# Kernel optimization log

Hardware: AMD Instinct MI355X
Metric: run time of the kernel (lower is better)

## Reference

```python
import jax, jax.numpy as jnp
import numpy as np

N_NODES = 50000
N_EDGES = 640000
D = 128
BN_EPS = 1e-5


def setup_inputs() -> dict:
    key = jax.random.key(0)
    k1, k2, k3 = jax.random.split(key, 3)
    x = jax.random.normal(k1, (N_NODES, D), dtype=jnp.float32)
    # Glorot-ish weight for GCNConv linear
    W = jax.random.normal(k2, (D, D), dtype=jnp.float32) * (1.0 / np.sqrt(D))
    b = jnp.zeros((D,), dtype=jnp.float32)
    gamma = jnp.ones((D,), dtype=jnp.float32)
    beta = jnp.zeros((D,), dtype=jnp.float32)
    edge_index = jax.random.randint(k3, (2, N_EDGES), 0, N_NODES, dtype=jnp.int64)
    return {"x": x, "W": W, "b": b, "gamma": gamma, "beta": beta, "edge_index": edge_index}


def reference(x, W, b, gamma, beta, edge_index):
    N = x.shape[0]
    # --- GCNConv: x' = D^{-1/2} (A + I) D^{-1/2} (x W) + b ---
    xw = x @ W  # [N, D]
    loops = jnp.arange(N, dtype=edge_index.dtype)
    src = jnp.concatenate([edge_index[0], loops])  # [E+N]
    dst = jnp.concatenate([edge_index[1], loops])
    ones = jnp.ones(src.shape[0], dtype=x.dtype)
    deg = jax.ops.segment_sum(ones, dst, num_segments=N)  # in-degree incl. self-loop
    dinv = jnp.where(deg > 0, jax.lax.rsqrt(deg), 0.0)
    norm = dinv[src] * dinv[dst]  # [E+N]
    msg = xw[src] * norm[:, None]  # [E+N, D] gathered + scaled messages
    h = jax.ops.segment_sum(msg, dst, num_segments=N) + b  # scatter-add aggregation
    # --- BatchNorm1d (training-mode batch stats over nodes, biased var) ---
    mean = jnp.mean(h, axis=0)
    var = jnp.mean(jnp.square(h - mean), axis=0)
    h = (h - mean) * jax.lax.rsqrt(var + BN_EPS) * gamma + beta
    # --- activation (relu) ---
    h = jax.nn.relu(h)
    # --- residual (in_channels == out_channels) ---
    h = x + h
    # --- dropout: identity in eval mode for deterministic reference ---
    return h
```

## Files before the change

### kernel.cpp

```cpp
#include <hip/hip_runtime.h>

#define DCH 128
#define ROWS 16
#define BN_EPS 1e-5f

typedef unsigned short u16;
typedef __attribute__((ext_vector_type(8))) short short8;
typedef __attribute__((ext_vector_type(4))) float floatx4;
typedef __attribute__((ext_vector_type(2))) unsigned uint2v;

__device__ __forceinline__ float bf2f(u16 u) {
    return __uint_as_float(((unsigned)u) << 16);
}
__device__ __forceinline__ u16 f2bf(float f) {
    unsigned u = __float_as_uint(f);
    u += 0x7FFFu + ((u >> 16) & 1u);
    return (u16)(u >> 16);
}
__device__ __forceinline__ float ldf(const void* p, int i, int isbf) {
    return isbf ? bf2f(((const u16*)p)[i]) : ((const float*)p)[i];
}

__global__ void zero_kernel(float* p, int n) {
    int stride = gridDim.x * 256;
    for (int i = blockIdx.x * 256 + threadIdx.x; i < n; i += stride) p[i] = 0.f;
}

__global__ void paint_kernel(u16* out, int n, unsigned val) {
    int stride = gridDim.x * 256;
    for (int i = blockIdx.x * 256 + threadIdx.x; i < n; i += stride) out[i] = (u16)val;
}

__global__ void prep_deg_kernel(const int* ei, int E, const u16* xw, int* ws_i,
                                const void* W, u16* Wb, int* deg, int N) {
    int t = threadIdx.x;
    __shared__ int s_nz, s_hits;
    if (t == 0) { s_nz = 0; s_hits = 0; }
    __syncthreads();
    int ewords = 2 * E;
    int nz = 0;
    for (int i = t; i < 1024; i += 256) {
        int w = 2 * i + 1;
        if (w < ewords) nz |= ei[w];
    }
    if (nz) atomicOr(&s_nz, 1);
    unsigned m = (xw[2 * t] >> 8) & 0x7F;
    if (m >= 0x3B && m <= 0x43) atomicAdd(&s_hits, 1);
    __syncthreads();
    int is64 = (s_nz == 0) ? 1 : 0;
    int isbf = (s_hits >= 128) ? 1 : 0;
    if (blockIdx.x == 0 && t == 0) {
        ws_i[0] = is64;
        ws_i[1] = isbf;
    }
    int gid = blockIdx.x * 256 + t;
    int gthreads = gridDim.x * 256;
    for (int idx = gid; idx < DCH * DCH; idx += gthreads) {
        int j = idx & 7, lane = (idx >> 3) & 63, kk = (idx >> 9) & 3, nt = idx >> 11;
        int k = kk * 32 + (lane >> 4) * 8 + j;
        int n = nt * 16 + (lane & 15);
        Wb[idx] = f2bf(ldf(W, k * DCH + n, isbf));
    }
    if (is64 && !(E & 1)) {
        int P2 = E >> 1;
        for (int p = gid; p < P2; p += gthreads) {
            int4 sp = ((const int4*)ei)[p];
            int4 dp = ((const int4*)(ei + 2 * E))[p];
            if (((unsigned)sp.x >= (unsigned)N) || ((unsigned)dp.x >= (unsigned)N) ||
                ((unsigned)sp.z >= (unsigned)N) || ((unsigned)dp.z >= (unsigned)N))
                atomicOr(&ws_i[2], 2);
            atomicAdd(&deg[min(max(dp.x, 0), N - 1)], 1);
            atomicAdd(&deg[min(max(dp.z, 0), N - 1)], 1);
        }
    } else {
        for (int e = gid; e < E; e += gthreads) {
            int s = is64 ? ei[2 * e] : ei[e];
            int d = is64 ? ei[2 * E + 2 * e] : ei[E + e];
            if (((unsigned)s >= (unsigned)N) || ((unsigned)d >= (unsigned)N))
                atomicOr(&ws_i[2], 2);
            atomicAdd(&deg[min(max(d, 0), N - 1)], 1);
        }
    }
}

__global__ void detect_kernel(const int* ei, int ewords, const u16* xw, int* ws_i) {
    __shared__ int s_nz, s_hits;
    int t = threadIdx.x;
    if (t == 0) { s_nz = 0; s_hits = 0; }
    __syncthreads();
    int nz = 0;
    for (int i = t; i < 1024; i += 256) {
        int w = 2 * i + 1;
        if (w < ewords) nz |= ei[w];
    }
    if (nz) atomicOr(&s_nz, 1);
    unsigned m = (xw[2 * t] >> 8) & 0x7F;
    if (m >= 0x3B && m <= 0x43) atomicAdd(&s_hits, 1);
    __syncthreads();
    if (t == 0) {
        ws_i[0] = (s_nz == 0) ? 1 : 0;
        ws_i[1] = (s_hits >= 128) ? 1 : 0;
        ws_i[2] = 0;
    }
}

__global__ void deg_kernel(const int* ei, int E, int* ws_i, int* deg, int N) {
    int is64 = ws_i[0];
    int i = blockIdx.x * 256 + threadIdx.x;
    if (i < E) {
        int s = is64 ? ei[2 * i] : ei[i];
        int d = is64 ? ei[2 * E + 2 * i] : ei[E + i];
        if (((unsigned)s >= (unsigned)N) || ((unsigned)d >= (unsigned)N))
            atomicOr(&ws_i[2], 2);
        d = min(max(d, 0), N - 1);
        atomicAdd(&deg[d], 1);
    }
}

__global__ void dinv_kernel(const int* deg, float* dinv, int N, int* ws_i) {
    int i = blockIdx.x * 256 + threadIdx.x;
    if (i < N) {
        float v = rsqrtf((float)(deg[i] + 1));
        if (!(v > 0.f && v <= 1.001f)) atomicOr(&ws_i[2], 4);
        dinv[i] = v;
    }
}

__global__ void scanA_kernel(const int* deg, int* part, int N) {
    int base = blockIdx.x * 1024 + threadIdx.x * 4;
    int s = 0;
    #pragma unroll
    for (int j = 0; j < 4; ++j) {
        int i = base + j;
        if (i < N) s += deg[i];
    }
    #pragma unroll
    for (int o = 1; o < 64; o <<= 1) s += __shfl_xor(s, o, 64);
    __shared__ int ws4[4];
    if ((threadIdx.x & 63) == 0) ws4[threadIdx.x >> 6] = s;
    __syncthreads();
    if (threadIdx.x == 0) part[blockIdx.x] = ws4[0] + ws4[1] + ws4[2] + ws4[3];
}

__global__ void scanC_kernel(int* deg_cursor, const int* part, int* rowptr,
                             float* dinv, int N, int P) {
    __shared__ int wsum[4], wsP[4];
    int t = threadIdx.x, lane = t & 63, w = t >> 6;
    int pv = (t < P && t < (int)blockIdx.x) ? part[t] : 0;
    #pragma unroll
    for (int o = 1; o < 64; o <<= 1) pv += __shfl_xor(pv, o, 64);
    if (lane == 0) wsP[w] = pv;

    int base = blockIdx.x * 1024 + t * 4;
    int v[4], ts = 0;
    #pragma unroll
    for (int j = 0; j < 4; ++j) {
        int i = base + j;
        v[j] = (i < N) ? deg_cursor[i] : 0;
        ts += v[j];
    }
    int sc = ts;
    #pragma unroll
    for (int o = 1; o < 64; o <<= 1) {
        int u = __shfl_up(sc, o, 64);
        if (lane >= o) sc += u;
    }
    if (lane == 63) wsum[w] = sc;
    __syncthreads();
    if (t < 4) {
        int s = wsum[t];
        #pragma unroll
        for (int o = 1; o < 4; o <<= 1) {
            int u = __shfl_up(s, o, 4);
            if (t >= o) s += u;
        }
        wsum[t] = s;
    }
    __syncthreads();
    int blockbase = wsP[0] + wsP[1] + wsP[2] + wsP[3];
    int run = sc - ts + (w ? wsum[w - 1] : 0) + blockbase;
    #pragma unroll
    for (int j = 0; j < 4; ++j) {
        int i = base + j;
        if (i < N) {
            deg_cursor[i] = run;
            run += v[j];
            rowptr[i + 1] = run;
            dinv[i] = rsqrtf((float)(v[j] + 1));
        }
    }
    if (blockIdx.x == 0 && t == 0) rowptr[0] = 0;
}

__global__ void fillcsr_kernel(const int* ei, int E, const int* ws_i,
                               int* cursor, int* col, int N) {
    int is64 = ws_i[0];
    int i = blockIdx.x * 256 + threadIdx.x;
    if (is64 && !(E & 1)) {
        if (2 * i < E) {
            int4 sp = ((const int4*)ei)[i];
            int4 dp = ((const int4*)(ei + 2 * E))[i];
            int s0 = min(max(sp.x, 0), N - 1), d0 = min(max(dp.x, 0), N - 1);
            int s1 = min(max(sp.z, 0), N - 1), d1 = min(max(dp.z, 0), N - 1);
            int p0 = atomicAdd(&cursor[d0], 1);
            if ((unsigned)p0 < (unsigned)E) col[p0] = s0;
            int p1 = atomicAdd(&cursor[d1], 1);
            if ((unsigned)p1 < (unsigned)E) col[p1] = s1;
        }
    } else if (i < E) {
        int s = is64 ? ei[2 * i] : ei[i];
        int d = is64 ? ei[2 * E + 2 * i] : ei[E + i];
        s = min(max(s, 0), N - 1);
        d = min(max(d, 0), N - 1);
        int pos = atomicAdd(&cursor[d], 1);
        if ((unsigned)pos < (unsigned)E) col[pos] = s;
    }
}

__global__ void gemm_mfma_kernel(const void* x, const u16* Wb, const float* dinv,
                                 const int* ws_i, u16* y, int N) {
    int isbf = ws_i[1];
    int t = threadIdx.x;
    int wv = t >> 6, lane = t & 63;
    int quad = lane >> 4, l16 = lane & 15;
    int r0 = blockIdx.x * 64 + wv * 16;
    int rl = min(r0 + l16, N - 1);
    short8 a[4];
    if (isbf) {
        const u16* xp = (const u16*)x + (size_t)rl * DCH + quad * 8;
        #pragma unroll
        for (int kk = 0; kk < 4; ++kk)
            a[kk] = *(const short8*)(xp + kk * 32);
    } else {
        const float* xp = (const float*)x + (size_t)rl * DCH + quad * 8;
        #pragma unroll
        for (int kk = 0; kk < 4; ++kk) {
            float4 f0 = *(const float4*)(xp + kk * 32);
            float4 f1 = *(const float4*)(xp + kk * 32 + 4);
            short8 aa;
            aa[0] = (short)f2bf(f0.x); aa[1] = (short)f2bf(f0.y);
            aa[2] = (short)f2bf(f0.z); aa[3] = (short)f2bf(f0.w);
            aa[4] = (short)f2bf(f1.x); aa[5] = (short)f2bf(f1.y);
            aa[6] = (short)f2bf(f1.z); aa[7] = (short)f2bf(f1.w);
            a[kk] = aa;
        }
    }
    floatx4 acc[8];
    #pragma unroll
    for (int i = 0; i < 8; ++i) acc[i] = (floatx4)(0.f);
    #pragma unroll
    for (int nt = 0; nt < 8; ++nt) {
        #pragma unroll
        for (int kk = 0; kk < 4; ++kk) {
            short8 bfr = *(const short8*)&Wb[(((nt << 2) | kk) * 64 + lane) * 8];
            acc[nt] = __builtin_amdgcn_mfma_f32_16x16x32_bf16(a[kk], bfr, acc[nt], 0, 0, 0);
        }
    }
    #pragma unroll
    for (int i = 0; i < 4; ++i) {
        int row = r0 + quad * 4 + i;
        if (row < N) {
            float dv = dinv[row];
            #pragma unroll
            for (int nt = 0; nt < 8; ++nt)
                y[(size_t)row * DCH + nt * 16 + l16] = f2bf(acc[nt][i] * dv);
        }
    }
}

__global__ __launch_bounds__(256, 4)
void gather_stats_kernel(const int* rowptr, const int* col, const u16* y,
                         const float* dinv, const void* b, const int* ws_i,
                         float* h, float* sums, float* sumsq, int N) {
    int isbf = ws_i[1];
    int t = threadIdx.x;
    int hw = t >> 5;
    int l32 = t & 31;
    int c0 = l32 * 4;
    float bb[4];
    #pragma unroll
    for (int k = 0; k < 4; ++k) bb[k] = ldf(b, c0 + k, isbf);
    float ps[4] = {0.f, 0.f, 0.f, 0.f}, pq[4] = {0.f, 0.f, 0.f, 0.f};
    int stream_id = blockIdx.x * 8 + hw;
    int nstreams = gridDim.x * 8;

    int n = stream_id;
    int beg = 0, end = 0;
    uint2v qs = (uint2v)(0u);
    if (n < N) {
        beg = rowptr[n];
        end = rowptr[n + 1];
        qs = *(const uint2v*)&y[(size_t)n * DCH + c0];
    }
    while (n < N) {
        int n2 = n + nstreams;
        int begN = 0, endN = 0;
        uint2v qsN = (uint2v)(0u);
        if (n2 < N) {
            begN = rowptr[n2];
            endN = rowptr[n2 + 1];
            qsN = *(const uint2v*)&y[(size_t)n2 * DCH + c0];
        }

        float a0[4] = { bf2f((u16)(qs.x & 0xFFFF)), bf2f((u16)(qs.x >> 16)),
                        bf2f((u16)(qs.y & 0xFFFF)), bf2f((u16)(qs.y >> 16)) };
        float a1[4] = {0.f, 0.f, 0.f, 0.f};
        float a2[4] = {0.f, 0.f, 0.f, 0.f};
        float a3[4] = {0.f, 0.f, 0.f, 0.f};
        int j = beg;
        int s0 = 0, s1 = 0, s2 = 0, s3 = 0, s4 = 0, s5 = 0, s6 = 0, s7 = 0;
        bool have8 = (j + 7 < end);
        if (have8) {
            s0 = __builtin_nontemporal_load(col + j);
            s1 = __builtin_nontemporal_load(col + j + 1);
            s2 = __builtin_nontemporal_load(col + j + 2);
            s3 = __builtin_nontemporal_load(col + j + 3);
            s4 = __builtin_nontemporal_load(col + j + 4);
            s5 = __builtin_nontemporal_load(col + j + 5);
            s6 = __builtin_nontemporal_load(col + j + 6);
            s7 = __builtin_nontemporal_load(col + j + 7);
        }
        while (have8) {
            uint2v q0 = *(const uint2v*)&y[(size_t)s0 * DCH + c0];
            uint2v q1 = *(const uint2v*)&y[(size_t)s1 * DCH + c0];
            uint2v q2 = *(const uint2v*)&y[(size_t)s2 * DCH + c0];
            uint2v q3 = *(const uint2v*)&y[(size_t)s3 * DCH + c0];
            uint2v q4 = *(const uint2v*)&y[(size_t)s4 * DCH + c0];
            uint2v q5 = *(const uint2v*)&y[(size_t)s5 * DCH + c0];
            uint2v q6 = *(const uint2v*)&y[(size_t)s6 * DCH + c0];
            uint2v q7 = *(const uint2v*)&y[(size_t)s7 * DCH + c0];
            int jn = j + 8;
            bool haven = (jn + 7 < end);
            if (haven) {
                s0 = __builtin_nontemporal_load(col + jn);
                s1 = __builtin_nontemporal_load(col + jn + 1);
                s2 = __builtin_nontemporal_load(col + jn + 2);
                s3 = __builtin_nontemporal_load(col + jn + 3);
                s4 = __builtin_nontemporal_load(col + jn + 4);
                s5 = __builtin_nontemporal_load(col + jn + 5);
                s6 = __builtin_nontemporal_load(col + jn + 6);
                s7 = __builtin_nontemporal_load(col + jn + 7);
            }
            a0[0] += bf2f((u16)(q0.x & 0xFFFF)); a0[1] += bf2f((u16)(q0.x >> 16));
            a0[2] += bf2f((u16)(q0.y & 0xFFFF)); a0[3] += bf2f((u16)(q0.y >> 16));
            a1[0] += bf2f((u16)(q1.x & 0xFFFF)); a1[1] += bf2f((u16)(q1.x >> 16));
            a1[2] += bf2f((u16)(q1.y & 0xFFFF)); a1[3] += bf2f((u16)(q1.y >> 16));
            a2[0] += bf2f((u16)(q2.x & 0xFFFF)); a2[1] += bf2f((u16)(q2.x >> 16));
            a2[2] += bf2f((u16)(q2.y & 0xFFFF)); a2[3] += bf2f((u16)(q2.y >> 16));
            a3[0] += bf2f((u16)(q3.x & 0xFFFF)); a3[1] += bf2f((u16)(q3.x >> 16));
            a3[2] += bf2f((u16)(q3.y & 0xFFFF)); a3[3] += bf2f((u16)(q3.y >> 16));
            a0[0] += bf2f((u16)(q4.x & 0xFFFF)); a0[1] += bf2f((u16)(q4.x >> 16));
            a0[2] += bf2f((u16)(q4.y & 0xFFFF)); a0[3] += bf2f((u16)(q4.y >> 16));
            a1[0] += bf2f((u16)(q5.x & 0xFFFF)); a1[1] += bf2f((u16)(q5.x >> 16));
            a1[2] += bf2f((u16)(q5.y & 0xFFFF)); a1[3] += bf2f((u16)(q5.y >> 16));
            a2[0] += bf2f((u16)(q6.x & 0xFFFF)); a2[1] += bf2f((u16)(q6.x >> 16));
            a2[2] += bf2f((u16)(q6.y & 0xFFFF)); a2[3] += bf2f((u16)(q6.y >> 16));
            a3[0] += bf2f((u16)(q7.x & 0xFFFF)); a3[1] += bf2f((u16)(q7.x >> 16));
            a3[2] += bf2f((u16)(q7.y & 0xFFFF)); a3[3] += bf2f((u16)(q7.y >> 16));
            j = jn; have8 = haven;
        }
        if (j + 3 < end) {
            s0 = __builtin_nontemporal_load(col + j);
            s1 = __builtin_nontemporal_load(col + j + 1);
            s2 = __builtin_nontemporal_load(col + j + 2);
            s3 = __builtin_nontemporal_load(col + j + 3);
            uint2v q0 = *(const uint2v*)&y[(size_t)s0 * DCH + c0];
            uint2v q1 = *(const uint2v*)&y[(size_t)s1 * DCH + c0];
            uint2v q2 = *(const uint2v*)&y[(size_t)s2 * DCH + c0];
            uint2v q3 = *(const uint2v*)&y[(size_t)s3 * DCH + c0];
            a0[0] += bf2f((u16)(q0.x & 0xFFFF)); a0[1] += bf2f((u16)(q0.x >> 16));
            a0[2] += bf2f((u16)(q0.y & 0xFFFF)); a0[3] += bf2f((u16)(q0.y >> 16));
            a1[0] += bf2f((u16)(q1.x & 0xFFFF)); a1[1] += bf2f((u16)(q1.x >> 16));
            a1[2] += bf2f((u16)(q1.y & 0xFFFF)); a1[3] += bf2f((u16)(q1.y >> 16));
            a2[0] += bf2f((u16)(q2.x & 0xFFFF)); a2[1] += bf2f((u16)(q2.x >> 16));
            a2[2] += bf2f((u16)(q2.y & 0xFFFF)); a2[3] += bf2f((u16)(q2.y >> 16));
            a3[0] += bf2f((u16)(q3.x & 0xFFFF)); a3[1] += bf2f((u16)(q3.x >> 16));
            a3[2] += bf2f((u16)(q3.y & 0xFFFF)); a3[3] += bf2f((u16)(q3.y >> 16));
            j += 4;
        }
        for (; j < end; ++j) {
            uint2v q0 = *(const uint2v*)&y[(size_t)__builtin_nontemporal_load(col + j) * DCH + c0];
            a0[0] += bf2f((u16)(q0.x & 0xFFFF)); a0[1] += bf2f((u16)(q0.x >> 16));
            a0[2] += bf2f((u16)(q0.y & 0xFFFF)); a0[3] += bf2f((u16)(q0.y >> 16));
        }
        float dn = dinv[n];
        floatx4 o;
        o[0] = fmaf((a0[0] + a1[0]) + (a2[0] + a3[0]), dn, bb[0]);
        o[1] = fmaf((a0[1] + a1[1]) + (a2[1] + a3[1]), dn, bb[1]);
        o[2] = fmaf((a0[2] + a1[2]) + (a2[2] + a3[2]), dn, bb[2]);
        o[3] = fmaf((a0[3] + a1[3]) + (a2[3] + a3[3]), dn, bb[3]);
        __builtin_nontemporal_store(o, (floatx4*)&h[(size_t)n * DCH + c0]);
        ps[0] += o[0]; pq[0] += o[0] * o[0];
        ps[1] += o[1]; pq[1] += o[1] * o[1];
        ps[2] += o[2]; pq[2] += o[2] * o[2];
        ps[3] += o[3]; pq[3] += o[3] * o[3];

        n = n2; beg = begN; end = endN; qs = qsN;
    }
    __shared__ float lps[8][DCH], lpq[8][DCH];
    #pragma unroll
    for (int k = 0; k < 4; ++k) { lps[hw][c0 + k] = ps[k]; lpq[hw][c0 + k] = pq[k]; }
    __syncthreads();
    if (t < DCH) {
        int ch = (t + blockIdx.x * 16) & 127;
        float s = 0.f, q = 0.f;
        #pragma unroll
        for (int i = 0; i < 8; ++i) { s += lps[i][ch]; q += lpq[i][ch]; }
        atomicAdd(&sums[ch], s);
        atomicAdd(&sumsq[ch], q);
    }
}

__global__ void gemm_valu_kernel(const void* x, const void* W, const float* dinv,
                                 const int* ws_i, void* y, int N) {
    __shared__ float WsF[64 * DCH];
    __shared__ float xs[ROWS * DCH];
    int isbf = ws_i[1];
    int t = threadIdx.x;
    int r0 = blockIdx.x * ROWS;
    for (int i = t; i < ROWS * DCH; i += 256) {
        int r = r0 + (i >> 7);
        xs[i] = (r < N) ? ldf(x, r * DCH + (i & 127), isbf) : 0.f;
    }
    int d = t & 127, rh = t >> 7;
    float s[8];
    #pragma unroll
    for (int j = 0; j < 8; ++j) s[j] = 0.f;
    for (int half = 0; half < 2; ++half) {
        __syncthreads();
        for (int i = t; i < 64 * DCH; i += 256)
            WsF[i] = ldf(W, half * 64 * DCH + i, isbf);
        __syncthreads();
        #pragma unroll
        for (int j = 0; j < 8; ++j) {
            int rr = rh + 2 * j;
            float a = s[j];
            #pragma unroll 16
            for (int k = 0; k < 64; ++k)
                a = fmaf(xs[rr * DCH + half * 64 + k], WsF[k * DCH + d], a);
            s[j] = a;
        }
    }
    #pragma unroll
    for (int j = 0; j < 8; ++j) {
        int r = r0 + rh + 2 * j;
        if (r < N) {
            float v = s[j] * dinv[r];
            if (isbf) ((u16*)y)[r * DCH + d] = f2bf(v);
            else      ((float*)y)[r * DCH + d] = v;
        }
    }
}

__global__ void scatter_kernel(const int* ei, int E, const int* ws_i,
                               const void* y, float* acc, int N) {
    int is64 = ws_i[0], isbf = ws_i[1];
    int gid = blockIdx.x * 256 + threadIdx.x;
    int e = gid >> 5;
    if (e >= E) return;
    int c0 = (gid & 31) * 4;
    int s = is64 ? ei[2 * e] : ei[e];
    int d = is64 ? ei[2 * E + 2 * e] : ei[E + e];
    s = min(max(s, 0), N - 1);
    d = min(max(d, 0), N - 1);
    float v0, v1, v2, v3;
    if (isbf) {
        uint2 raw = *(const uint2*)&((const u16*)y)[s * DCH + c0];
        v0 = bf2f((u16)(raw.x & 0xFFFF)); v1 = bf2f((u16)(raw.x >> 16));
        v2 = bf2f((u16)(raw.y & 0xFFFF)); v3 = bf2f((u16)(raw.y >> 16));
    } else {
        float4 raw = *(const float4*)&((const float*)y)[s * DCH + c0];
        v0 = raw.x; v1 = raw.y; v2 = raw.z; v3 = raw.w;
    }
    float* a = &acc[d * DCH + c0];
    atomicAdd(a + 0, v0);
    atomicAdd(a + 1, v1);
    atomicAdd(a + 2, v2);
    atomicAdd(a + 3, v3);
}

__global__ void bnstat_kernel(const void* y, float* acc, const float* dinv,
                              const void* b, int* ws_i,
                              float* sums, float* sumsq, int total) {
    int isbf = ws_i[1];
    int t = threadIdx.x;
    int d = t & 127;
    float bb = ldf(b, d, isbf);
    float ps = 0.f, pq = 0.f;
    int stride = gridDim.x * 256;
    for (int i = blockIdx.x * 256 + t; i < total; i += stride) {
        int r = i >> 7;
        float yv = isbf ? bf2f(((const u16*)y)[i]) : ((const float*)y)[i];
        float v = (yv + acc[i]) * dinv[r] + bb;
        acc[i] = v;
        ps += v;
        pq += v * v;
    }
    __shared__ float ls[256], lq[256];
    ls[t] = ps; lq[t] = pq;
    __syncthreads();
    if (t < 128) {
        atomicAdd(&sums[d], ls[t] + ls[t + 128]);
        atomicAdd(&sumsq[d], lq[t] + lq[t + 128]);
    }
}

__global__ void out_kernel(const float* h, const void* x,
                           const void* gamma, const void* beta,
                           int* ws_i, const float* sums, const float* sumsq,
                           void* out, int total, float invN) {
    __shared__ float sc[DCH], sh[DCH];
    int isbf = ws_i[1];
    int t = threadIdx.x;
    if (t < DCH) {
        float mean = sums[t] * invN;
        float var = fmaxf(sumsq[t] * invN - mean * mean, 0.f);
        float s = ldf(gamma, t, isbf) * rsqrtf(var + BN_EPS);
        if (!(var < 1e8f && fabsf(s) < 1e6f)) atomicOr(&ws_i[2], 32);
        sc[t] = s;
        sh[t] = ldf(beta, t, isbf) - mean * s;
    }
    __syncthreads();
    int total4 = total >> 2;
    int stride = gridDim.x * 256;
    int i0 = blockIdx.x * 256 + t;
    int d0 = (i0 << 2) & 127;
    float c0 = sc[d0], c1 = sc[d0 + 1], c2 = sc[d0 + 2], c3 = sc[d0 + 3];
    float f0 = sh[d0], f1 = sh[d0 + 1], f2 = sh[d0 + 2], f3 = sh[d0 + 3];
    if (isbf) {
        for (int i = i0; i < total4; i += stride) {
            floatx4 hv = __builtin_nontemporal_load((const floatx4*)h + i);
            uint2v xv = __builtin_nontemporal_load((const uint2v*)x + i);
            float v0 = fmaxf(fmaf(hv[0], c0, f0), 0.f) + bf2f((u16)(xv.x & 0xFFFF));
            float v1 = fmaxf(fmaf(hv[1], c1, f1), 0.f) + bf2f((u16)(xv.x >> 16));
            float v2 = fmaxf(fmaf(hv[2], c2, f2), 0.f) + bf2f((u16)(xv.y & 0xFFFF));
            float v3 = fmaxf(fmaf(hv[3], c3, f3), 0.f) + bf2f((u16)(xv.y >> 16));
            uint2v o;
            o.x = (unsigned)f2bf(v0) | ((unsigned)f2bf(v1) << 16);
            o.y = (unsigned)f2bf(v2) | ((unsigned)f2bf(v3) << 16);
            __builtin_nontemporal_store(o, (uint2v*)out + i);
        }
    } else {
        for (int i = i0; i < total4; i += stride) {
            floatx4 hv = __builtin_nontemporal_load((const floatx4*)h + i);
            floatx4 xv = __builtin_nontemporal_load((const floatx4*)x + i);
            floatx4 o;
            o[0] = fmaxf(fmaf(hv[0], c0, f0), 0.f) + xv[0];
            o[1] = fmaxf(fmaf(hv[1], c1, f1), 0.f) + xv[1];
            o[2] = fmaxf(fmaf(hv[2], c2, f2), 0.f) + xv[2];
            o[3] = fmaxf(fmaf(hv[3], c3, f3), 0.f) + xv[3];
            __builtin_nontemporal_store(o, (floatx4*)out + i);
        }
    }
    for (int i = (total4 << 2) + i0; i < total; i += stride) {
        int d = i & 127;
        float v = fmaxf(fmaf(h[i], sc[d], sh[d]), 0.f);
        if (isbf) ((u16*)out)[i] = f2bf(v + bf2f(((const u16*)x)[i]));
        else      ((float*)out)[i] = v + ((const float*)x)[i];
    }
}

__global__ void diag_kernel(const int* ws_i, void* out, int n) {
    int e = ws_i[2];
    if (!e) return;
    int isbf = ws_i[1];
    float v = 4096.f + 32.f * (float)(e & 63);
    int stride = gridDim.x * 256;
    if (isbf) {
        u16 code = f2bf(v);
        for (int i = blockIdx.x * 256 + threadIdx.x; i < n; i += stride)
            ((u16*)out)[i] = code;
    } else {
        for (int i = blockIdx.x * 256 + threadIdx.x; i < n; i += stride)
            ((float*)out)[i] = v;
    }
}

extern "C" void kernel_launch(void* const* d_in, const int* in_sizes, int n_in,
                              void* d_out, int out_size, void* d_ws, size_t ws_size,
                              hipStream_t stream) {
    const void* x     = d_in[0];
    const void* W     = d_in[1];
    const void* b     = d_in[2];
    const void* gamma = d_in[3];
    const void* beta  = d_in[4];
    const int*  ei    = (const int*)d_in[5];

    const int N  = in_sizes[0] / DCH;
    const int E  = in_sizes[5] / 2;
    const int ND = N * DCH;
    const int P  = (N + 1023) / 1024;

    char* wsb = (char*)d_ws;
    int*  ws_i = (int*)wsb;

    size_t o_wb   = 64;
    size_t o_deg  = o_wb + 32768;
    size_t o_sum  = o_deg + 4 * (size_t)N;
    size_t o_sq   = o_sum + 512;
    size_t o_rp   = o_sq + 512;
    size_t o_dinv = o_rp + 4 * ((size_t)N + 1) + 4;
    size_t o_part = o_dinv + 4 * (size_t)N;
    size_t o_h    = (o_part + 1024 + 255) & ~(size_t)255;
    size_t o_col  = o_h + 4 * (size_t)ND;
    size_t need_csr = o_col + 4 * (size_t)E;

    (void)hipGetLastError();

    if (ws_size >= need_csr && P <= 256) {
        u16*   Wb    = (u16*)(wsb + o_wb);
        int*   deg   = (int*)(wsb + o_deg);
        float* sums  = (float*)(wsb + o_sum);
        float* sumsq = (float*)(wsb + o_sq);
        int*   rowptr= (int*)(wsb + o_rp);
        float* dinv  = (float*)(wsb + o_dinv);
        int*   part  = (int*)(wsb + o_part);
        float* h     = (float*)(wsb + o_h);
        int*   col   = (int*)(wsb + o_col);
        u16*   y     = (u16*)d_out;

        zero_kernel<<<128, 256, 0, stream>>>((float*)wsb, (int)((o_sq + 512) / 4));
        prep_deg_kernel<<<1250, 256, 0, stream>>>(ei, E, (const u16*)x, ws_i,
                                                  W, Wb, deg, N);
        scanA_kernel<<<P, 256, 0, stream>>>(deg, part, N);
        scanC_kernel<<<P, 256, 0, stream>>>(deg, part, rowptr, dinv, N, P);
        fillcsr_kernel<<<(E + 255) / 256, 256, 0, stream>>>(ei, E, ws_i, deg, col, N);
        gemm_mfma_kernel<<<(N + 63) / 64, 256, 0, stream>>>(x, Wb, dinv, ws_i, y, N);
        gather_stats_kernel<<<1024, 256, 0, stream>>>(rowptr, col, y, dinv, b, ws_i,
                                                      h, sums, sumsq, N);
        out_kernel<<<2048, 256, 0, stream>>>(h, x, gamma, beta, ws_i, sums, sumsq,
                                             d_out, ND, 1.0f / (float)N);
        diag_kernel<<<512, 256, 0, stream>>>(ws_i, d_out, out_size);
    } else {
        int*   deg   = (int*)(wsb + 16);
        float* dinv  = (float*)(wsb + 16 + 4 * (size_t)N);
        float* sums  = (float*)(wsb + 16 + 8 * (size_t)N);
        float* sumsq = sums + DCH;
        float* acc   = sumsq + DCH;
        size_t need = 16 + 8 * (size_t)N + 1024 + 4 * (size_t)ND;
        if (ws_size < need) {
            int mb = (int)(ws_size >> 20); if (mb > 127) mb = 127;
            float v = 2048.f + 16.f * (float)mb;
            unsigned u; __builtin_memcpy(&u, &v, 4);
            paint_kernel<<<1024, 256, 0, stream>>>((u16*)d_out, out_size, u >> 16);
            return;
        }
        detect_kernel<<<1, 256, 0, stream>>>(ei, 2 * E, (const u16*)x, ws_i);
        zero_kernel<<<2048, 256, 0, stream>>>((float*)(wsb + 16), 2 * N + 256 + ND);
        deg_kernel<<<(E + 255) / 256, 256, 0, stream>>>(ei, E, ws_i, deg, N);
        dinv_kernel<<<(N + 255) / 256, 256, 0, stream>>>(deg, dinv, N, ws_i);
        gemm_valu_kernel<<<(N + ROWS - 1) / ROWS, 256, 0, stream>>>(x, W, dinv, ws_i, d_out, N);
        scatter_kernel<<<(E * 32 + 255) / 256, 256, 0, stream>>>(ei, E, ws_i, d_out, acc, N);
        bnstat_kernel<<<240, 256, 0, stream>>>(d_out, acc, dinv, b, ws_i, sums, sumsq, ND);
        out_kernel<<<256, 256, 0, stream>>>(acc, x, gamma, beta, ws_i, sums, sumsq,
                                            d_out, ND, 1.0f / (float)N);
        diag_kernel<<<512, 256, 0, stream>>>(ws_i, d_out, out_size);
    }

    if (hipGetLastError() != hipSuccess)
        hipMemsetAsync(d_out, 0x42, (size_t)out_size * 2, stream);
}
```

Before: 237.5 us.

## Merge scan into one block, co-launch CSR fill with GEMM, fold diag into output

Replaces the two-kernel multi-block scan with a single 1024-thread block scan and fuses the CSR fill and the MFMA GEMM into one launch, split by block index. The diagnostic fill is folded into the output kernel, which now reads the error flag once into shared memory. Together these remove three kernel launches and let the independent fill and GEMM work run at the same time. The cost is a serial single-block scan over 50k nodes and heavier branch-divergent blocks in the merged kernel.

```diff
diff --git a/kernel.cpp b/kernel.cpp
--- a/kernel.cpp
+++ b/kernel.cpp
@@ -126,144 +126,121 @@
     }
 }
 
-__global__ void scanA_kernel(const int* deg, int* part, int N) {
-    int base = blockIdx.x * 1024 + threadIdx.x * 4;
-    int s = 0;
-    #pragma unroll
-    for (int j = 0; j < 4; ++j) {
-        int i = base + j;
-        if (i < N) s += deg[i];
-    }
-    #pragma unroll
-    for (int o = 1; o < 64; o <<= 1) s += __shfl_xor(s, o, 64);
-    __shared__ int ws4[4];
-    if ((threadIdx.x & 63) == 0) ws4[threadIdx.x >> 6] = s;
-    __syncthreads();
-    if (threadIdx.x == 0) part[blockIdx.x] = ws4[0] + ws4[1] + ws4[2] + ws4[3];
-}
-
-__global__ void scanC_kernel(int* deg_cursor, const int* part, int* rowptr,
-                             float* dinv, int N, int P) {
-    __shared__ int wsum[4], wsP[4];
-    int t = threadIdx.x, lane = t & 63, w = t >> 6;
-    int pv = (t < P && t < (int)blockIdx.x) ? part[t] : 0;
-    #pragma unroll
-    for (int o = 1; o < 64; o <<= 1) pv += __shfl_xor(pv, o, 64);
-    if (lane == 0) wsP[w] = pv;
-
-    int base = blockIdx.x * 1024 + t * 4;
-    int v[4], ts = 0;
-    #pragma unroll
-    for (int j = 0; j < 4; ++j) {
-        int i = base + j;
-        v[j] = (i < N) ? deg_cursor[i] : 0;
-        ts += v[j];
-    }
-    int sc = ts;
+__global__ void scan1_kernel(int* deg_cursor, int* rowptr, float* dinv, int N) {
+    int t = threadIdx.x, lane = t & 63, wv = t >> 6;
+    int C = (N + 1023) >> 10;
+    int base = t * C;
+    int lsum = 0;
+    for (int k = 0; k < C; ++k) {
+        int i = base + k;
+        if (i < N) lsum += deg_cursor[i];
+    }
+    int inc = lsum;
     #pragma unroll
     for (int o = 1; o < 64; o <<= 1) {
-        int u = __shfl_up(sc, o, 64);
-        if (lane >= o) sc += u;
-    }
-    if (lane == 63) wsum[w] = sc;
-    __syncthreads();
-    if (t < 4) {
+        int u = __shfl_up(inc, o, 64);
+        if (lane >= o) inc += u;
+    }
+    __shared__ int wsum[16];
+    if (lane == 63) wsum[wv] = inc;
+    __syncthreads();
+    if (t < 16) {
         int s = wsum[t];
         #pragma unroll
-        for (int o = 1; o < 4; o <<= 1) {
-            int u = __shfl_up(s, o, 4);
+        for (int o = 1; o < 16; o <<= 1) {
+            int u = __shfl_up(s, o, 16);
             if (t >= o) s += u;
         }
         wsum[t] = s;
     }
     __syncthreads();
-    int blockbase = wsP[0] + wsP[1] + wsP[2] + wsP[3];
-    int run = sc - ts + (w ? wsum[w - 1] : 0) + blockbase;
-    #pragma unroll
-    for (int j = 0; j < 4; ++j) {
-        int i = base + j;
+    int run = inc - lsum + (wv ? wsum[wv - 1] : 0);
+    for (int k = 0; k < C; ++k) {
+        int i = base + k;
         if (i < N) {
+            int d = deg_cursor[i];
             deg_cursor[i] = run;
-            run += v[j];
+            run += d;
             rowptr[i + 1] = run;
-            dinv[i] = rsqrtf((float)(v[j] + 1));
-        }
-    }
-    if (blockIdx.x == 0 && t == 0) rowptr[0] = 0;
-}
-
-__global__ void fillcsr_kernel(const int* ei, int E, const int* ws_i,
-                               int* cursor, int* col, int N) {
-    int is64 = ws_i[0];
-    int i = blockIdx.x * 256 + threadIdx.x;
-    if (is64 && !(E & 1)) {
-        if (2 * i < E) {
-            int4 sp = ((const int4*)ei)[i];
-            int4 dp = ((const int4*)(ei + 2 * E))[i];
-            int s0 = min(max(sp.x, 0), N - 1), d0 = min(max(dp.x, 0), N - 1);
-            int s1 = min(max(sp.z, 0), N - 1), d1 = min(max(dp.z, 0), N - 1);
-            int p0 = atomicAdd(&cursor[d0], 1);
-            if ((unsigned)p0 < (unsigned)E) col[p0] = s0;
-            int p1 = atomicAdd(&cursor[d1], 1);
-            if ((unsigned)p1 < (unsigned)E) col[p1] = s1;
-        }
-    } else if (i < E) {
-        int s = is64 ? ei[2 * i] : ei[i];
-        int d = is64 ? ei[2 * E + 2 * i] : ei[E + i];
-        s = min(max(s, 0), N - 1);
-        d = min(max(d, 0), N - 1);
-        int pos = atomicAdd(&cursor[d], 1);
-        if ((unsigned)pos < (unsigned)E) col[pos] = s;
-    }
-}
-
-__global__ void gemm_mfma_kernel(const void* x, const u16* Wb, const float* dinv,
-                                 const int* ws_i, u16* y, int N) {
-    int isbf = ws_i[1];
+            dinv[i] = rsqrtf((float)(d + 1));
+        }
+    }
+    if (t == 0) rowptr[0] = 0;
+}
+
+__global__ void fill_gemm_kernel(const int* ei, int E, const int* ws_i,
+                                 int* cursor, int* col,
+                                 const void* x, const u16* Wb, const float* dinv,
+                                 u16* y, int N, int GB) {
     int t = threadIdx.x;
-    int wv = t >> 6, lane = t & 63;
-    int quad = lane >> 4, l16 = lane & 15;
-    int r0 = blockIdx.x * 64 + wv * 16;
-    int rl = min(r0 + l16, N - 1);
-    short8 a[4];
-    if (isbf) {
-        const u16* xp = (const u16*)x + (size_t)rl * DCH + quad * 8;
+    if ((int)blockIdx.x < GB) {
+        int isbf = ws_i[1];
+        int wv = t >> 6, lane = t & 63;
+        int quad = lane >> 4, l16 = lane & 15;
+        int r0 = blockIdx.x * 64 + wv * 16;
+        int rl = min(r0 + l16, N - 1);
+        short8 a[4];
+        if (isbf) {
+            const u16* xp = (const u16*)x + (size_t)rl * DCH + quad * 8;
+            #pragma unroll
+            for (int kk = 0; kk < 4; ++kk)
+                a[kk] = *(const short8*)(xp + kk * 32);
+        } else {
+            const float* xp = (const float*)x + (size_t)rl * DCH + quad * 8;
+            #pragma unroll
+            for (int kk = 0; kk < 4; ++kk) {
+                float4 f0 = *(const float4*)(xp + kk * 32);
+                float4 f1 = *(const float4*)(xp + kk * 32 + 4);
+                short8 aa;
+                aa[0] = (short)f2bf(f0.x); aa[1] = (short)f2bf(f0.y);
+                aa[2] = (short)f2bf(f0.z); aa[3] = (short)f2bf(f0.w);
+                aa[4] = (short)f2bf(f1.x); aa[5] = (short)f2bf(f1.y);
+                aa[6] = (short)f2bf(f1.z); aa[7] = (short)f2bf(f1.w);
+                a[kk] = aa;
+            }
+        }
+        floatx4 acc[8];
         #pragma unroll
-        for (int kk = 0; kk < 4; ++kk)
-            a[kk] = *(const short8*)(xp + kk * 32);
+        for (int i = 0; i < 8; ++i) acc[i] = (floatx4)(0.f);
+        #pragma unroll
+        for (int nt = 0; nt < 8; ++nt) {
+            #pragma unroll
+            for (int kk = 0; kk < 4; ++kk) {
+                short8 bfr = *(const short8*)&Wb[(((nt << 2) | kk) * 64 + lane) * 8];
+                acc[nt] = __builtin_amdgcn_mfma_f32_16x16x32_bf16(a[kk], bfr, acc[nt], 0, 0, 0);
+            }
+        }
+        #pragma unroll
+        for (int i = 0; i < 4; ++i) {
+            int row = r0 + quad * 4 + i;
+            if (row < N) {
+                float dv = dinv[row];
+                #pragma unroll
+                for (int nt = 0; nt < 8; ++nt)
+                    y[(size_t)row * DCH + nt * 16 + l16] = f2bf(acc[nt][i] * dv);
+            }
+        }
     } else {
-        const float* xp = (const float*)x + (size_t)rl * DCH + quad * 8;
-        #pragma unroll
-        for (int kk = 0; kk < 4; ++kk) {
-            float4 f0 = *(const float4*)(xp + kk * 32);
-            float4 f1 = *(const float4*)(xp + kk * 32 + 4);
-            short8 aa;
-            aa[0] = (short)f2bf(f0.x); aa[1] = (short)f2bf(f0.y);
-            aa[2] = (short)f2bf(f0.z); aa[3] = (short)f2bf(f0.w);
-            aa[4] = (short)f2bf(f1.x); aa[5] = (short)f2bf(f1.y);
-            aa[6] = (short)f2bf(f1.z); aa[7] = (short)f2bf(f1.w);
-            a[kk] = aa;
-        }
-    }
-    floatx4 acc[8];
-    #pragma unroll
-    for (int i = 0; i < 8; ++i) acc[i] = (floatx4)(0.f);
-    #pragma unroll
-    for (int nt = 0; nt < 8; ++nt) {
-        #pragma unroll
-        for (int kk = 0; kk < 4; ++kk) {
-            short8 bfr = *(const short8*)&Wb[(((nt << 2) | kk) * 64 + lane) * 8];
-            acc[nt] = __builtin_amdgcn_mfma_f32_16x16x32_bf16(a[kk], bfr, acc[nt], 0, 0, 0);
-        }
-    }
-    #pragma unroll
-    for (int i = 0; i < 4; ++i) {
-        int row = r0 + quad * 4 + i;
-        if (row < N) {
-            float dv = dinv[row];
-            #pragma unroll
-            for (int nt = 0; nt < 8; ++nt)
-                y[(size_t)row * DCH + nt * 16 + l16] = f2bf(acc[nt][i] * dv);
+        int is64 = ws_i[0];
+        int i = (blockIdx.x - GB) * 256 + t;
+        if (is64 && !(E & 1)) {
+            if (2 * i < E) {
+                int4 sp = ((const int4*)ei)[i];
+                int4 dp = ((const int4*)(ei + 2 * E))[i];
+                int s0 = min(max(sp.x, 0), N - 1), d0 = min(max(dp.x, 0), N - 1);
+                int s1 = min(max(sp.z, 0), N - 1), d1 = min(max(dp.z, 0), N - 1);
+                int p0 = atomicAdd(&cursor[d0], 1);
+                if ((unsigned)p0 < (unsigned)E) col[p0] = s0;
+                int p1 = atomicAdd(&cursor[d1], 1);
+                if ((unsigned)p1 < (unsigned)E) col[p1] = s1;
+            }
+        } else if (i < E) {
+            int s = is64 ? ei[2 * i] : ei[i];
+            int d = is64 ? ei[2 * E + 2 * i] : ei[E + i];
+            s = min(max(s, 0), N - 1);
+            d = min(max(d, 0), N - 1);
+            int pos = atomicAdd(&cursor[d], 1);
+            if ((unsigned)pos < (unsigned)E) col[pos] = s;
         }
     }
 }
@@ -510,19 +487,35 @@
                            int* ws_i, const float* sums, const float* sumsq,
                            void* out, int total, float invN) {
     __shared__ float sc[DCH], sh[DCH];
+    __shared__ int s_bad;
     int isbf = ws_i[1];
     int t = threadIdx.x;
+    if (t == 0) s_bad = ws_i[2];
+    __syncthreads();
     if (t < DCH) {
         float mean = sums[t] * invN;
         float var = fmaxf(sumsq[t] * invN - mean * mean, 0.f);
         float s = ldf(gamma, t, isbf) * rsqrtf(var + BN_EPS);
-        if (!(var < 1e8f && fabsf(s) < 1e6f)) atomicOr(&ws_i[2], 32);
+        if (!(var < 1e8f && fabsf(s) < 1e6f)) atomicOr(&s_bad, 32);
         sc[t] = s;
         sh[t] = ldf(beta, t, isbf) - mean * s;
     }
     __syncthreads();
+    int e = s_bad;
+    int stride = gridDim.x * 256;
+    if (e) {
+        float v = 4096.f + 32.f * (float)(e & 63);
+        if (isbf) {
+            u16 code = f2bf(v);
+            for (int i = blockIdx.x * 256 + t; i < total; i += stride)
+                ((u16*)out)[i] = code;
+        } else {
+            for (int i = blockIdx.x * 256 + t; i < total; i += stride)
+                ((float*)out)[i] = v;
+        }
+        return;
+    }
     int total4 = total >> 2;
-    int stride = gridDim.x * 256;
     int i0 = blockIdx.x * 256 + t;
     int d0 = (i0 << 2) & 127;
     float c0 = sc[d0], c1 = sc[d0 + 1], c2 = sc[d0 + 2], c3 = sc[d0 + 3];
@@ -560,22 +553,6 @@
     }
 }
 
-__global__ void diag_kernel(const int* ws_i, void* out, int n) {
-    int e = ws_i[2];
-    if (!e) return;
-    int isbf = ws_i[1];
-    float v = 4096.f + 32.f * (float)(e & 63);
-    int stride = gridDim.x * 256;
-    if (isbf) {
-        u16 code = f2bf(v);
-        for (int i = blockIdx.x * 256 + threadIdx.x; i < n; i += stride)
-            ((u16*)out)[i] = code;
-    } else {
-        for (int i = blockIdx.x * 256 + threadIdx.x; i < n; i += stride)
-            ((float*)out)[i] = v;
-    }
-}
-
 extern "C" void kernel_launch(void* const* d_in, const int* in_sizes, int n_in,
                               void* d_out, int out_size, void* d_ws, size_t ws_size,
                               hipStream_t stream) {
@@ -589,7 +566,6 @@
     const int N  = in_sizes[0] / DCH;
     const int E  = in_sizes[5] / 2;
     const int ND = N * DCH;
-    const int P  = (N + 1023) / 1024;
 
     char* wsb = (char*)d_ws;
     int*  ws_i = (int*)wsb;
@@ -607,30 +583,30 @@
 
     (void)hipGetLastError();
 
-    if (ws_size >= need_csr && P <= 256) {
+    if (ws_size >= need_csr) {
         u16*   Wb    = (u16*)(wsb + o_wb);
         int*   deg   = (int*)(wsb + o_deg);
         float* sums  = (float*)(wsb + o_sum);
         float* sumsq = (float*)(wsb + o_sq);
         int*   rowptr= (int*)(wsb + o_rp);
         float* dinv  = (float*)(wsb + o_dinv);
-        int*   part  = (int*)(wsb + o_part);
         float* h     = (float*)(wsb + o_h);
         int*   col   = (int*)(wsb + o_col);
         u16*   y     = (u16*)d_out;
 
+        int GB = (N + 63) / 64;
+        int FB = (E + 255) / 256;
+
         zero_kernel<<<128, 256, 0, stream>>>((float*)wsb, (int)((o_sq + 512) / 4));
         prep_deg_kernel<<<1250, 256, 0, stream>>>(ei, E, (const u16*)x, ws_i,
                                                   W, Wb, deg, N);
-        scanA_kernel<<<P, 256, 0, stream>>>(deg, part, N);
-        scanC_kernel<<<P, 256, 0, stream>>>(deg, part, rowptr, dinv, N, P);
-        fillcsr_kernel<<<(E + 255) / 256, 256, 0, stream>>>(ei, E, ws_i, deg, col, N);
-        gemm_mfma_kernel<<<(N + 63) / 64, 256, 0, stream>>>(x, Wb, dinv, ws_i, y, N);
+        scan1_kernel<<<1, 1024, 0, stream>>>(deg, rowptr, dinv, N);
+        fill_gemm_kernel<<<GB + FB, 256, 0, stream>>>(ei, E, ws_i, deg, col,
+                                                      x, Wb, dinv, y, N, GB);
         gather_stats_kernel<<<1024, 256, 0, stream>>>(rowptr, col, y, dinv, b, ws_i,
                                                       h, sums, sumsq, N);
         out_kernel<<<2048, 256, 0, stream>>>(h, x, gamma, beta, ws_i, sums, sumsq,
                                              d_out, ND, 1.0f / (float)N);
-        diag_kernel<<<512, 256, 0, stream>>>(ws_i, d_out, out_size);
     } else {
         int*   deg   = (int*)(wsb + 16);
         float* dinv  = (float*)(wsb + 16 + 4 * (size_t)N);
@@ -654,7 +630,6 @@
         bnstat_kernel<<<240, 256, 0, stream>>>(d_out, acc, dinv, b, ws_i, sums, sumsq, ND);
         out_kernel<<<256, 256, 0, stream>>>(acc, x, gamma, beta, ws_i, sums, sumsq,
                                             d_out, ND, 1.0f / (float)N);
-        diag_kernel<<<512, 256, 0, stream>>>(ws_i, d_out, out_size);
     }
 
     if (hipGetLastError() != hipSuccess)
```

Result: slower. 370.8 us (+56.2%).

## Merge CSR fill with GEMM launch and fold diagnostic fill into output kernel

Applied to the files above, without the earlier changes.

Merges the CSR column fill and the MFMA GEMM into one launch whose blocks split by index, so the two independent stages can run concurrently on the GPU. Also removes the separate diagnostic kernel by checking the error flag inside the output kernel and painting the error code there. This cuts two kernel launches and lets the atomic-heavy fill overlap with the GEMM, at the cost of mixing heterogeneous block types and their register footprints in one kernel. The in-block error check now reads ws_i[2] once per block and no longer writes the flag back globally.

```diff
diff --git a/kernel.cpp b/kernel.cpp
--- a/kernel.cpp
+++ b/kernel.cpp
@@ -192,78 +192,79 @@
     if (blockIdx.x == 0 && t == 0) rowptr[0] = 0;
 }
 
-__global__ void fillcsr_kernel(const int* ei, int E, const int* ws_i,
-                               int* cursor, int* col, int N) {
-    int is64 = ws_i[0];
-    int i = blockIdx.x * 256 + threadIdx.x;
-    if (is64 && !(E & 1)) {
-        if (2 * i < E) {
-            int4 sp = ((const int4*)ei)[i];
-            int4 dp = ((const int4*)(ei + 2 * E))[i];
-            int s0 = min(max(sp.x, 0), N - 1), d0 = min(max(dp.x, 0), N - 1);
-            int s1 = min(max(sp.z, 0), N - 1), d1 = min(max(dp.z, 0), N - 1);
-            int p0 = atomicAdd(&cursor[d0], 1);
-            if ((unsigned)p0 < (unsigned)E) col[p0] = s0;
-            int p1 = atomicAdd(&cursor[d1], 1);
-            if ((unsigned)p1 < (unsigned)E) col[p1] = s1;
-        }
-    } else if (i < E) {
-        int s = is64 ? ei[2 * i] : ei[i];
-        int d = is64 ? ei[2 * E + 2 * i] : ei[E + i];
-        s = min(max(s, 0), N - 1);
-        d = min(max(d, 0), N - 1);
-        int pos = atomicAdd(&cursor[d], 1);
-        if ((unsigned)pos < (unsigned)E) col[pos] = s;
-    }
-}
-
-__global__ void gemm_mfma_kernel(const void* x, const u16* Wb, const float* dinv,
-                                 const int* ws_i, u16* y, int N) {
-    int isbf = ws_i[1];
+__global__ void fill_gemm_kernel(const int* ei, int E, const int* ws_i,
+                                 int* cursor, int* col,
+                                 const void* x, const u16* Wb, const float* dinv,
+                                 u16* y, int N, int GB) {
     int t = threadIdx.x;
-    int wv = t >> 6, lane = t & 63;
-    int quad = lane >> 4, l16 = lane & 15;
-    int r0 = blockIdx.x * 64 + wv * 16;
-    int rl = min(r0 + l16, N - 1);
-    short8 a[4];
-    if (isbf) {
-        const u16* xp = (const u16*)x + (size_t)rl * DCH + quad * 8;
+    if ((int)blockIdx.x < GB) {
+        int isbf = ws_i[1];
+        int wv = t >> 6, lane = t & 63;
+        int quad = lane >> 4, l16 = lane & 15;
+        int r0 = blockIdx.x * 64 + wv * 16;
+        int rl = min(r0 + l16, N - 1);
+        short8 a[4];
+        if (isbf) {
+            const u16* xp = (const u16*)x + (size_t)rl * DCH + quad * 8;
+            #pragma unroll
+            for (int kk = 0; kk < 4; ++kk)
+                a[kk] = *(const short8*)(xp + kk * 32);
+        } else {
+            const float* xp = (const float*)x + (size_t)rl * DCH + quad * 8;
+            #pragma unroll
+            for (int kk = 0; kk < 4; ++kk) {
+                float4 f0 = *(const float4*)(xp + kk * 32);
+                float4 f1 = *(const float4*)(xp + kk * 32 + 4);
+                short8 aa;
+                aa[0] = (short)f2bf(f0.x); aa[1] = (short)f2bf(f0.y);
+                aa[2] = (short)f2bf(f0.z); aa[3] = (short)f2bf(f0.w);
+                aa[4] = (short)f2bf(f1.x); aa[5] = (short)f2bf(f1.y);
+                aa[6] = (short)f2bf(f1.z); aa[7] = (short)f2bf(f1.w);
+                a[kk] = aa;
+            }
+        }
+        floatx4 acc[8];
         #pragma unroll
-        for (int kk = 0; kk < 4; ++kk)
-            a[kk] = *(const short8*)(xp + kk * 32);
+        for (int i = 0; i < 8; ++i) acc[i] = (floatx4)(0.f);
+        #pragma unroll
+        for (int nt = 0; nt < 8; ++nt) {
+            #pragma unroll
+            for (int kk = 0; kk < 4; ++kk) {
+                short8 bfr = *(const short8*)&Wb[(((nt << 2) | kk) * 64 + lane) * 8];
+                acc[nt] = __builtin_amdgcn_mfma_f32_16x16x32_bf16(a[kk], bfr, acc[nt], 0, 0, 0);
+            }
+        }
+        #pragma unroll
+        for (int i = 0; i < 4; ++i) {
+            int row = r0 + quad * 4 + i;
+            if (row < N) {
+                float dv = dinv[row];
+                #pragma unroll
+                for (int nt = 0; nt < 8; ++nt)
+                    y[(size_t)row * DCH + nt * 16 + l16] = f2bf(acc[nt][i] * dv);
+            }
+        }
     } else {
-        const float* xp = (const float*)x + (size_t)rl * DCH + quad * 8;
-        #pragma unroll
-        for (int kk = 0; kk < 4; ++kk) {
-            float4 f0 = *(const float4*)(xp + kk * 32);
-            float4 f1 = *(const float4*)(xp + kk * 32 + 4);
-            short8 aa;
-            aa[0] = (short)f2bf(f0.x); aa[1] = (short)f2bf(f0.y);
-            aa[2] = (short)f2bf(f0.z); aa[3] = (short)f2bf(f0.w);
-            aa[4] = (short)f2bf(f1.x); aa[5] = (short)f2bf(f1.y);
-            aa[6] = (short)f2bf(f1.z); aa[7] = (short)f2bf(f1.w);
-            a[kk] = aa;
-        }
-    }
-    floatx4 acc[8];
-    #pragma unroll
-    for (int i = 0; i < 8; ++i) acc[i] = (floatx4)(0.f);
-    #pragma unroll
-    for (int nt = 0; nt < 8; ++nt) {
-        #pragma unroll
-        for (int kk = 0; kk < 4; ++kk) {
-            short8 bfr = *(const short8*)&Wb[(((nt << 2) | kk) * 64 + lane) * 8];
-            acc[nt] = __builtin_amdgcn_mfma_f32_16x16x32_bf16(a[kk], bfr, acc[nt], 0, 0, 0);
-        }
-    }
-    #pragma unroll
-    for (int i = 0; i < 4; ++i) {
-        int row = r0 + quad * 4 + i;
-        if (row < N) {
-            float dv = dinv[row];
-            #pragma unroll
-            for (int nt = 0; nt < 8; ++nt)
-                y[(size_t)row * DCH + nt * 16 + l16] = f2bf(acc[nt][i] * dv);
+        int is64 = ws_i[0];
+        int i = (blockIdx.x - GB) * 256 + t;
+        if (is64 && !(E & 1)) {
+            if (2 * i < E) {
+                int4 sp = ((const int4*)ei)[i];
+                int4 dp = ((const int4*)(ei + 2 * E))[i];
+                int s0 = min(max(sp.x, 0), N - 1), d0 = min(max(dp.x, 0), N - 1);
+                int s1 = min(max(sp.z, 0), N - 1), d1 = min(max(dp.z, 0), N - 1);
+                int p0 = atomicAdd(&cursor[d0], 1);
+                if ((unsigned)p0 < (unsigned)E) col[p0] = s0;
+                int p1 = atomicAdd(&cursor[d1], 1);
+                if ((unsigned)p1 < (unsigned)E) col[p1] = s1;
+            }
+        } else if (i < E) {
+            int s = is64 ? ei[2 * i] : ei[i];
+            int d = is64 ? ei[2 * E + 2 * i] : ei[E + i];
+            s = min(max(s, 0), N - 1);
+            d = min(max(d, 0), N - 1);
+            int pos = atomicAdd(&cursor[d], 1);
+            if ((unsigned)pos < (unsigned)E) col[pos] = s;
         }
     }
 }
@@ -510,19 +511,35 @@
                            int* ws_i, const float* sums, const float* sumsq,
                            void* out, int total, float invN) {
     __shared__ float sc[DCH], sh[DCH];
+    __shared__ int s_bad;
     int isbf = ws_i[1];
     int t = threadIdx.x;
+    if (t == 0) s_bad = ws_i[2];
+    __syncthreads();
     if (t < DCH) {
         float mean = sums[t] * invN;
         float var = fmaxf(sumsq[t] * invN - mean * mean, 0.f);
         float s = ldf(gamma, t, isbf) * rsqrtf(var + BN_EPS);
-        if (!(var < 1e8f && fabsf(s) < 1e6f)) atomicOr(&ws_i[2], 32);
+        if (!(var < 1e8f && fabsf(s) < 1e6f)) atomicOr(&s_bad, 32);
         sc[t] = s;
         sh[t] = ldf(beta, t, isbf) - mean * s;
     }
     __syncthreads();
+    int e = s_bad;
+    int stride = gridDim.x * 256;
+    if (e) {
+        float v = 4096.f + 32.f * (float)(e & 63);
+        if (isbf) {
+            u16 code = f2bf(v);
+            for (int i = blockIdx.x * 256 + t; i < total; i += stride)
+                ((u16*)out)[i] = code;
+        } else {
+            for (int i = blockIdx.x * 256 + t; i < total; i += stride)
+                ((float*)out)[i] = v;
+        }
+        return;
+    }
     int total4 = total >> 2;
-    int stride = gridDim.x * 256;
     int i0 = blockIdx.x * 256 + t;
     int d0 = (i0 << 2) & 127;
     float c0 = sc[d0], c1 = sc[d0 + 1], c2 = sc[d0 + 2], c3 = sc[d0 + 3];
@@ -560,22 +577,6 @@
     }
 }
 
-__global__ void diag_kernel(const int* ws_i, void* out, int n) {
-    int e = ws_i[2];
-    if (!e) return;
-    int isbf = ws_i[1];
-    float v = 4096.f + 32.f * (float)(e & 63);
-    int stride = gridDim.x * 256;
-    if (isbf) {
-        u16 code = f2bf(v);
-        for (int i = blockIdx.x * 256 + threadIdx.x; i < n; i += stride)
-            ((u16*)out)[i] = code;
-    } else {
-        for (int i = blockIdx.x * 256 + threadIdx.x; i < n; i += stride)
-            ((float*)out)[i] = v;
-    }
-}
-
 extern "C" void kernel_launch(void* const* d_in, const int* in_sizes, int n_in,
                               void* d_out, int out_size, void* d_ws, size_t ws_size,
                               hipStream_t stream) {
@@ -619,18 +620,20 @@
         int*   col   = (int*)(wsb + o_col);
         u16*   y     = (u16*)d_out;
 
+        int GB = (N + 63) / 64;
+        int FB = (E + 255) / 256;
+
         zero_kernel<<<128, 256, 0, stream>>>((float*)wsb, (int)((o_sq + 512) / 4));
         prep_deg_kernel<<<1250, 256, 0, stream>>>(ei, E, (const u16*)x, ws_i,
                                                   W, Wb, deg, N);
         scanA_kernel<<<P, 256, 0, stream>>>(deg, part, N);
         scanC_kernel<<<P, 256, 0, stream>>>(deg, part, rowptr, dinv, N, P);
-        fillcsr_kernel<<<(E + 255) / 256, 256, 0, stream>>>(ei, E, ws_i, deg, col, N);
-        gemm_mfma_kernel<<<(N + 63) / 64, 256, 0, stream>>>(x, Wb, dinv, ws_i, y, N);
+        fill_gemm_kernel<<<GB + FB, 256, 0, stream>>>(ei, E, ws_i, deg, col,
+                                                      x, Wb, dinv, y, N, GB);
         gather_stats_kernel<<<1024, 256, 0, stream>>>(rowptr, col, y, dinv, b, ws_i,
                                                       h, sums, sumsq, N);
         out_kernel<<<2048, 256, 0, stream>>>(h, x, gamma, beta, ws_i, sums, sumsq,
                                              d_out, ND, 1.0f / (float)N);
-        diag_kernel<<<512, 256, 0, stream>>>(ws_i, d_out, out_size);
     } else {
         int*   deg   = (int*)(wsb + 16);
         float* dinv  = (float*)(wsb + 16 + 4 * (size_t)N);
@@ -654,7 +657,6 @@
         bnstat_kernel<<<240, 256, 0, stream>>>(d_out, acc, dinv, b, ws_i, sums, sumsq, ND);
         out_kernel<<<256, 256, 0, stream>>>(acc, x, gamma, beta, ws_i, sums, sumsq,
                                             d_out, ND, 1.0f / (float)N);
-        diag_kernel<<<512, 256, 0, stream>>>(ws_i, d_out, out_size);
     }
 
     if (hipGetLastError() != hipSuccess)
```

Measured after the change: 235.9 us. About the same (-0.6%).
